# Performance work log

Hardware: AMD Instinct MI355X
Metric: run time of the kernel (lower is better)

The kernel has to match this reference:

```python
import jax, jax.numpy as jnp
import numpy as np


def setup_inputs() -> dict:
    key = jax.random.key(0)
    k1, k2, k3 = jax.random.split(key, 3)
    x = jax.random.normal(k1, (128, 3, 16, 64, 64), dtype=jnp.float32)
    conv_weight = jax.random.normal(k2, (24, 3, 3, 3, 3), dtype=jnp.float32) * 0.1
    conv_bias = jax.random.normal(k3, (24,), dtype=jnp.float32) * 0.1
    return {"x": x, "conv_weight": conv_weight, "conv_bias": conv_bias}


def reference(x, conv_weight, conv_bias):
    # Conv3d, stride=1, padding=0 (VALID), dilation=1, groups=1, NCDHW layout
    y = jax.lax.conv_general_dilated(
        x, conv_weight,
        window_strides=(1, 1, 1),
        padding='VALID',
        dimension_numbers=('NCDHW', 'OIDHW', 'NCDHW'),
    )
    y = y + conv_bias[None, :, None, None, None]  # [B, 24, 14, 62, 62]
    y = jnp.min(y, axis=2)                        # min over depth -> [B, 24, 62, 62]
    return jax.nn.softmax(y, axis=1)              # softmax over channels
```

## Files before the change

### kernel.cpp

```cpp
#include <hip/hip_runtime.h>
#include <math.h>

#define CIN   3
#define DIN   16
#define HWIN  64
#define COUT  24
#define DOUT  14
#define HOUT  62
#define WOUT  62

#define TILE_H  4
#define NTILES  16
#define NTHR    512
#define ROWS_IN 6
#define RP      68
#define PLANE_F (CIN * ROWS_IN * RP)
#define XSLAB_F (DIN * PLANE_F)
#define WOFF    XSLAB_F
#define WT_F    324
#define LDS_F   (XSLAB_F + 8 * WT_F)
#define SM_RP     64
#define SM_STRIDE (TILE_H * SM_RP)


__device__ __forceinline__ void gload_lds_dw(const float* g, float* l) {
    __builtin_amdgcn_global_load_lds(
        (const __attribute__((address_space(1))) unsigned int*)g,
        (__attribute__((address_space(3))) unsigned int*)l, 4, 0, 0);
}

template<int C>
__device__ __forceinline__ void do_chunk(const float* __restrict__ xv,
                                         const float* __restrict__ wqb,
                                         float (&m)[3][4], const int p0)
{
    float acc[C][3][4];
    #pragma unroll
    for (int d = 0; d < C; ++d)
        #pragma unroll
        for (int cop = 0; cop < 3; ++cop)
            #pragma unroll
            for (int i = 0; i < 4; ++i) acc[d][cop][i] = 0.f;

    #pragma unroll 1
    for (int cin = 0; cin < CIN; ++cin) {
        #pragma unroll 1
        for (int kh = 0; kh < 3; ++kh) {
            const float* __restrict__ bp = xv + p0 * PLANE_F + cin * (ROWS_IN * RP) + kh * RP;
            const float* __restrict__ wp = wqb + (cin * 3 + kh) * 36;

            float4 wv[9];
            #pragma unroll
            for (int t = 0; t < 9; ++t) wv[t] = *(const float4*)(wp + t * 4);

            #pragma unroll
            for (int pp = 0; pp < C + 2; ++pp) {
                const float* rp2 = bp + pp * PLANE_F;
                const float4 a4 = *(const float4*)rp2;
                const float2 a2 = *(const float2*)(rp2 + 4);
                const float xr[6] = { a4.x, a4.y, a4.z, a4.w, a2.x, a2.y };
                #pragma unroll
                for (int kd = 0; kd < 3; ++kd) {
                    const int d = pp - kd;
                    if (d < 0 || d >= C) continue;
                    #pragma unroll
                    for (int kw = 0; kw < 3; ++kw) {
                        const float4 wt = wv[kd * 3 + kw];
                        const float wc[3] = { wt.x, wt.y, wt.z };
                        #pragma unroll
                        for (int cop = 0; cop < 3; ++cop)
                            #pragma unroll
                            for (int i = 0; i < 4; ++i)
                                acc[d][cop][i] = fmaf(wc[cop], xr[i + kw], acc[d][cop][i]);
                    }
                }
            }
        }
    }

    #pragma unroll
    for (int d = 0; d < C; ++d)
        #pragma unroll
        for (int cop = 0; cop < 3; ++cop)
            #pragma unroll
            for (int i = 0; i < 4; ++i)
                m[cop][i] = fminf(m[cop][i], acc[d][cop][i]);
}

__global__ __launch_bounds__(NTHR, 2) void conv_min_softmax_v7(
    const float* __restrict__ x,
    const float* __restrict__ w,
    const float* __restrict__ bias,
    float* __restrict__ out)
{
    __shared__ __align__(16) float smem[LDS_F];

    const int tid  = threadIdx.x;
    const int bid  = blockIdx.x;
    const int rt   = bid & (NTILES - 1);
    const int b    = bid >> 4;

    const int q    = __builtin_amdgcn_readfirstlane(tid >> 6);
    const int lane = tid & 63;
    const int r    = lane >> 4;
    const int wg   = lane & 15;
    const int q3   = q * 3;

    for (int i = tid; i < COUT * 81; i += NTHR) {
        const int co   = i / 81;
        const int rem  = i % 81;
        const int cin  = rem / 27;
        const int rem2 = rem % 27;
        const int kd   = rem2 / 9;
        const int kh   = (rem2 % 9) / 3;
        const int kw   = rem2 % 3;
        smem[WOFF + (co / 3) * WT_F + (cin * 3 + kh) * 36 + (kd * 3 + kw) * 4 + (co % 3)] = w[i];
    }
    const float bia[3] = { bias[q3 + 0], bias[q3 + 1], bias[q3 + 2] };

    {
        const float* __restrict__ xb =
            x + (size_t)b * (CIN * DIN * HWIN * HWIN) + lane;
        #pragma unroll
        for (int k = 0; k < 36; ++k) {
            const int p    = 2 * q + (k >= 18 ? 1 : 0);
            const int sub  = k % 18;
            const int cin  = sub / 6;
            const int row  = sub % 6;
            const int grow = min(rt * TILE_H + row, HWIN - 1);
            gload_lds_dw(xb + ((cin * DIN + p) * (HWIN * HWIN) + grow * HWIN),
                         &smem[p * PLANE_F + (cin * ROWS_IN + row) * RP]);
        }
    }
    __syncthreads();

    float m[3][4];
    #pragma unroll
    for (int cop = 0; cop < 3; ++cop)
        #pragma unroll
        for (int i = 0; i < 4; ++i) m[cop][i] = 1e30f;

    const float* __restrict__ xv  = &smem[r * RP + wg * 4];
    const float* __restrict__ wqb = &smem[WOFF + q * WT_F];

    do_chunk<4>(xv, wqb, m, 0);
    do_chunk<4>(xv, wqb, m, 4);
    do_chunk<3>(xv, wqb, m, 8);
    do_chunk<3>(xv, wqb, m, 11);

    __syncthreads();

    {
        const int p = r * SM_RP + wg * 4;
        #pragma unroll
        for (int cop = 0; cop < 3; ++cop) {
            float4 v = { m[cop][0] + bia[cop], m[cop][1] + bia[cop],
                         m[cop][2] + bia[cop], m[cop][3] + bia[cop] };
            *(float4*)&smem[(q3 + cop) * SM_STRIDE + p] = v;
        }
    }
    __syncthreads();

    if (tid < 256) {
        const int row = tid >> 6;
        const int col = tid & 63;
        const int ho  = rt * TILE_H + row;
        if (col < WOUT && ho < HOUT) {
            float v[COUT];
            float mx = -1e30f;
            #pragma unroll
            for (int c = 0; c < COUT; ++c) {
                v[c] = smem[c * SM_STRIDE + row * SM_RP + col];
                mx = fmaxf(mx, v[c]);
            }
            float s = 0.f;
            #pragma unroll
            for (int c = 0; c < COUT; ++c) { v[c] = __expf(v[c] - mx); s += v[c]; }
            const float inv = 1.f / s;
            float* ob = out + (size_t)b * COUT * (HOUT * WOUT) + ho * WOUT + col;
            #pragma unroll
            for (int c = 0; c < COUT; ++c)
                ob[(size_t)c * (HOUT * WOUT)] = v[c] * inv;
        }
    }
}

extern "C" void kernel_launch(void* const* d_in, const int* in_sizes, int n_in,
                              void* d_out, int out_size, void* d_ws, size_t ws_size,
                              hipStream_t stream) {
    const float* x    = (const float*)d_in[0];
    const float* w    = (const float*)d_in[1];
    const float* bias = (const float*)d_in[2];
    float* out = (float*)d_out;

    conv_min_softmax_v7<<<128 * NTILES, NTHR, 0, stream>>>(x, w, bias, out);
}
```

Baseline: 476.8 us.

## Use 6 waves with 4 output channels each and read weights from global

```diff
diff --git a/kernel.cpp b/kernel.cpp
--- a/kernel.cpp
+++ b/kernel.cpp
@@ -11,14 +11,12 @@
 
 #define TILE_H  4
 #define NTILES  16
-#define NTHR    512
+#define NTHR    384
 #define ROWS_IN 6
 #define RP      68
 #define PLANE_F (CIN * ROWS_IN * RP)
 #define XSLAB_F (DIN * PLANE_F)
-#define WOFF    XSLAB_F
-#define WT_F    324
-#define LDS_F   (XSLAB_F + 8 * WT_F)
+#define WQ_F    324
 #define SM_RP     64
 #define SM_STRIDE (TILE_H * SM_RP)
 
@@ -29,16 +27,30 @@
         (__attribute__((address_space(3))) unsigned int*)l, 4, 0, 0);
 }
 
+__global__ void repack_weights_v8(const float* __restrict__ w, float* __restrict__ ws) {
+    const int i = threadIdx.x + blockIdx.x * blockDim.x;
+    if (i < COUT * 81) {
+        const int co   = i / 81;
+        const int rem  = i % 81;
+        const int cin  = rem / 27;
+        const int rem2 = rem % 27;
+        const int kd   = rem2 / 9;
+        const int kh   = (rem2 % 9) / 3;
+        const int kw   = rem2 % 3;
+        ws[(co >> 2) * WQ_F + (cin * 3 + kh) * 36 + (kd * 3 + kw) * 4 + (co & 3)] = w[i];
+    }
+}
+
 template<int C>
 __device__ __forceinline__ void do_chunk(const float* __restrict__ xv,
-                                         const float* __restrict__ wqb,
-                                         float (&m)[3][4], const int p0)
+                                         const float* __restrict__ wsq,
+                                         float (&m)[4][4], const int p0)
 {
-    float acc[C][3][4];
+    float acc[C][4][4];
     #pragma unroll
     for (int d = 0; d < C; ++d)
         #pragma unroll
-        for (int cop = 0; cop < 3; ++cop)
+        for (int cop = 0; cop < 4; ++cop)
             #pragma unroll
             for (int i = 0; i < 4; ++i) acc[d][cop][i] = 0.f;
 
@@ -47,11 +59,12 @@
         #pragma unroll 1
         for (int kh = 0; kh < 3; ++kh) {
             const float* __restrict__ bp = xv + p0 * PLANE_F + cin * (ROWS_IN * RP) + kh * RP;
-            const float* __restrict__ wp = wqb + (cin * 3 + kh) * 36;
+            const int g = cin * 3 + kh;
 
             float4 wv[9];
             #pragma unroll
-            for (int t = 0; t < 9; ++t) wv[t] = *(const float4*)(wp + t * 4);
+            for (int t = 0; t < 9; ++t)
+                wv[t] = *(const float4*)(wsq + g * 36 + t * 4);
 
             #pragma unroll
             for (int pp = 0; pp < C + 2; ++pp) {
@@ -66,9 +79,9 @@
                     #pragma unroll
                     for (int kw = 0; kw < 3; ++kw) {
                         const float4 wt = wv[kd * 3 + kw];
-                        const float wc[3] = { wt.x, wt.y, wt.z };
+                        const float wc[4] = { wt.x, wt.y, wt.z, wt.w };
                         #pragma unroll
-                        for (int cop = 0; cop < 3; ++cop)
+                        for (int cop = 0; cop < 4; ++cop)
                             #pragma unroll
                             for (int i = 0; i < 4; ++i)
                                 acc[d][cop][i] = fmaf(wc[cop], xr[i + kw], acc[d][cop][i]);
@@ -81,19 +94,19 @@
     #pragma unroll
     for (int d = 0; d < C; ++d)
         #pragma unroll
-        for (int cop = 0; cop < 3; ++cop)
+        for (int cop = 0; cop < 4; ++cop)
             #pragma unroll
             for (int i = 0; i < 4; ++i)
                 m[cop][i] = fminf(m[cop][i], acc[d][cop][i]);
 }
 
-__global__ __launch_bounds__(NTHR, 2) void conv_min_softmax_v7(
+__global__ __launch_bounds__(NTHR, 3) void conv_min_softmax_v8(
     const float* __restrict__ x,
-    const float* __restrict__ w,
+    const float* __restrict__ ws,
     const float* __restrict__ bias,
     float* __restrict__ out)
 {
-    __shared__ __align__(16) float smem[LDS_F];
+    __shared__ __align__(16) float smem[XSLAB_F];
 
     const int tid  = threadIdx.x;
     const int bid  = blockIdx.x;
@@ -104,27 +117,18 @@
     const int lane = tid & 63;
     const int r    = lane >> 4;
     const int wg   = lane & 15;
-    const int q3   = q * 3;
-
-    for (int i = tid; i < COUT * 81; i += NTHR) {
-        const int co   = i / 81;
-        const int rem  = i % 81;
-        const int cin  = rem / 27;
-        const int rem2 = rem % 27;
-        const int kd   = rem2 / 9;
-        const int kh   = (rem2 % 9) / 3;
-        const int kw   = rem2 % 3;
-        smem[WOFF + (co / 3) * WT_F + (cin * 3 + kh) * 36 + (kd * 3 + kw) * 4 + (co % 3)] = w[i];
-    }
-    const float bia[3] = { bias[q3 + 0], bias[q3 + 1], bias[q3 + 2] };
+    const int q4   = q * 4;
+
+    const float bia[4] = { bias[q4 + 0], bias[q4 + 1], bias[q4 + 2], bias[q4 + 3] };
 
     {
         const float* __restrict__ xb =
             x + (size_t)b * (CIN * DIN * HWIN * HWIN) + lane;
-        #pragma unroll
-        for (int k = 0; k < 36; ++k) {
-            const int p    = 2 * q + (k >= 18 ? 1 : 0);
-            const int sub  = k % 18;
+        #pragma unroll 1
+        for (int k = 0; k < 48; ++k) {
+            const int j    = q * 48 + k;
+            const int p    = j / 18;
+            const int sub  = j % 18;
             const int cin  = sub / 6;
             const int row  = sub % 6;
             const int grow = min(rt * TILE_H + row, HWIN - 1);
@@ -134,29 +138,30 @@
     }
     __syncthreads();
 
-    float m[3][4];
+    float m[4][4];
     #pragma unroll
-    for (int cop = 0; cop < 3; ++cop)
+    for (int cop = 0; cop < 4; ++cop)
         #pragma unroll
         for (int i = 0; i < 4; ++i) m[cop][i] = 1e30f;
 
     const float* __restrict__ xv  = &smem[r * RP + wg * 4];
-    const float* __restrict__ wqb = &smem[WOFF + q * WT_F];
-
-    do_chunk<4>(xv, wqb, m, 0);
-    do_chunk<4>(xv, wqb, m, 4);
-    do_chunk<3>(xv, wqb, m, 8);
-    do_chunk<3>(xv, wqb, m, 11);
+    const float* __restrict__ wsq = ws + q * WQ_F;
+
+    do_chunk<3>(xv, wsq, m, 0);
+    do_chunk<3>(xv, wsq, m, 3);
+    do_chunk<3>(xv, wsq, m, 6);
+    do_chunk<3>(xv, wsq, m, 9);
+    do_chunk<2>(xv, wsq, m, 12);
 
     __syncthreads();
 
     {
         const int p = r * SM_RP + wg * 4;
         #pragma unroll
-        for (int cop = 0; cop < 3; ++cop) {
+        for (int cop = 0; cop < 4; ++cop) {
             float4 v = { m[cop][0] + bia[cop], m[cop][1] + bia[cop],
                          m[cop][2] + bia[cop], m[cop][3] + bia[cop] };
-            *(float4*)&smem[(q3 + cop) * SM_STRIDE + p] = v;
+            *(float4*)&smem[(q4 + cop) * SM_STRIDE + p] = v;
         }
     }
     __syncthreads();
@@ -192,6 +197,8 @@
     const float* w    = (const float*)d_in[1];
     const float* bias = (const float*)d_in[2];
     float* out = (float*)d_out;
-
-    conv_min_softmax_v7<<<128 * NTILES, NTHR, 0, stream>>>(x, w, bias, out);
-}
+    float* ws  = (float*)d_ws;
+
+    repack_weights_v8<<<8, 256, 0, stream>>>(w, ws);
+    conv_min_softmax_v8<<<128 * NTILES, NTHR, 0, stream>>>(x, ws, bias, out);
+}
```

Result: slower. 606.2 us (+27.1%).
